# Kernel tuning notes

Hardware: AMD Instinct MI355X
Metric: run time of the kernel (lower is better)

Reference implementation:

```python
import jax, jax.numpy as jnp
import numpy as np

N_NODES = 100000
N_EDGES = 1600000
D_FEAT = 64


def setup_inputs() -> dict:
    key = jax.random.key(0)
    k1, k2, k3 = jax.random.split(key, 3)
    x = jax.random.normal(k1, (N_NODES, D_FEAT), dtype=jnp.float32)
    edge_index = jax.random.randint(k2, (2, N_EDGES), 0, N_NODES, dtype=jnp.int64)
    edge_attr = jax.random.uniform(k3, (N_EDGES,), dtype=jnp.float32)
    return {"x": x, "edge_index": edge_index, "edge_attr": edge_attr}


def reference(x, edge_index, edge_attr):
    # out[row[i]] += exp(-edge_attr[i]) * x[col[i]]  for every edge i
    row, col = edge_index[0], edge_index[1]
    B = jnp.exp(-edge_attr)                      # [E] per-edge scalar kernel
    msgs = B[:, None] * x[col]                   # [E, D] gather + scale
    out = jax.ops.segment_sum(msgs, row, num_segments=N_NODES)  # scatter-add
    return out
```

## Files before the change

kernel.cpp:

```cpp
#include <hip/hip_runtime.h>
#include <math.h>

#define N_NODES_C 100000
#define D_FEAT 64

#define NB_F 512
#define FB_SHIFT 9
#define FB_MASK (NB_F - 1)
#define LMAX 256
#define CAP_E 4096
#define COL_BITS 17
#define COL_MASK17 0x1FFFF
#define NB_AGG 512
#define AGG_ITERS 8

__global__ void spline_scatter_atomic(const float* __restrict__ x,
                                      const int* __restrict__ row_idx,
                                      const int* __restrict__ col_idx,
                                      const float* __restrict__ edge_attr,
                                      float* __restrict__ out,
                                      int n_edges) {
    long long t = (long long)blockIdx.x * blockDim.x + threadIdx.x;
    int e = (int)(t >> 6);
    int f = (int)(t & 63);
    if (e >= n_edges) return;
    int r = row_idx[e];
    int c = col_idx[e];
    float w = expf(-edge_attr[e]);
    atomicAdd(&out[(long long)r * D_FEAT + f], w * x[(long long)c * D_FEAT + f]);
}


__global__ void hist_kernel(const int* __restrict__ row_idx, int* __restrict__ counts,
                            int n_edges) {
    int e = blockIdx.x * blockDim.x + threadIdx.x;
    if (e < n_edges) atomicAdd(&counts[row_idx[e]], 1);
}

__global__ void scan_kernel(const int* __restrict__ counts, int* __restrict__ start,
                            int* __restrict__ cursor, int n) {
    __shared__ int wave_sums[16];
    __shared__ int carry_s;
    const int tid = threadIdx.x;
    const int lane = tid & 63;
    const int wid = tid >> 6;
    if (tid == 0) carry_s = 0;
    __syncthreads();
    for (int base = 0; base < n; base += 1024) {
        int i = base + tid;
        int v = (i < n) ? counts[i] : 0;
        int inc = v;
        #pragma unroll
        for (int d = 1; d < 64; d <<= 1) {
            int t = __shfl_up(inc, d, 64);
            if (lane >= d) inc += t;
        }
        if (lane == 63) wave_sums[wid] = inc;
        __syncthreads();
        if (tid == 0) {
            int s = carry_s;
            #pragma unroll
            for (int k = 0; k < 16; ++k) { int t = wave_sums[k]; wave_sums[k] = s; s += t; }
            carry_s = s;
        }
        __syncthreads();
        int excl = inc - v + wave_sums[wid];
        if (i < n) { start[i] = excl; cursor[i] = excl; }
        __syncthreads();
    }
    if (tid == 0) start[n] = carry_s;
}

__global__ void bucket_kernel(const int* __restrict__ row_idx,
                              const int* __restrict__ col_idx,
                              const float* __restrict__ edge_attr,
                              int* __restrict__ cursor,
                              int2* __restrict__ colw,
                              int n_edges) {
    int e = blockIdx.x * blockDim.x + threadIdx.x;
    if (e >= n_edges) return;
    int r = row_idx[e];
    int c = col_idx[e];
    float w = expf(-edge_attr[e]);
    int pos = atomicAdd(&cursor[r], 1);
    colw[pos] = make_int2(c, __float_as_int(w));
}

__global__ void gather_accum_kernel(const float* __restrict__ x,
                                    const int* __restrict__ start,
                                    const int2* __restrict__ colw,
                                    float* __restrict__ out,
                                    int n_nodes) {
    int node = blockIdx.x * (blockDim.x >> 6) + (threadIdx.x >> 6);
    int lane = threadIdx.x & 63;
    if (node >= n_nodes) return;
    int b = start[node];
    int e = start[node + 1];
    float acc = 0.0f;
    int j = b;
    for (; j + 3 < e; j += 4) {
        int2 c0 = colw[j], c1 = colw[j + 1], c2 = colw[j + 2], c3 = colw[j + 3];
        acc += __int_as_float(c0.y) * x[(size_t)c0.x * D_FEAT + lane];
        acc += __int_as_float(c1.y) * x[(size_t)c1.x * D_FEAT + lane];
        acc += __int_as_float(c2.y) * x[(size_t)c2.x * D_FEAT + lane];
        acc += __int_as_float(c3.y) * x[(size_t)c3.x * D_FEAT + lane];
    }
    for (; j < e; ++j) {
        int2 c0 = colw[j];
        acc += __int_as_float(c0.y) * x[(size_t)c0.x * D_FEAT + lane];
    }
    out[(size_t)node * D_FEAT + lane] = acc;
}


__global__ void init_cursor_kernel(int* __restrict__ ccursor) {
    int i = blockIdx.x * blockDim.x + threadIdx.x;
    if (i < NB_F) ccursor[i] = i * CAP_E;
}

__global__ __launch_bounds__(512) void agg_scatter2_kernel(const int* __restrict__ row,
                                                           const int* __restrict__ col,
                                                           const float* __restrict__ attr,
                                                           int* __restrict__ ccursor,
                                                           int2* __restrict__ cw,
                                                           int n_edges, int chunk) {
    __shared__ int h[NB_F];
    __shared__ int gbase[NB_F];
    __shared__ int lcur[NB_F];
    const int tid = threadIdx.x;
    const int base = blockIdx.x * chunk;
    const int end = min(base + chunk, n_edges);
    h[tid] = 0;
    lcur[tid] = 0;
    __syncthreads();
    int rc[AGG_ITERS];
    #pragma unroll
    for (int k = 0; k < AGG_ITERS; ++k) {
        int e = base + k * 512 + tid;
        rc[k] = (e < end) ? row[e] : -1;
        if (rc[k] >= 0) atomicAdd(&h[rc[k] & FB_MASK], 1);
    }
    __syncthreads();
    {
        int c = h[tid];
        gbase[tid] = c ? atomicAdd(&ccursor[tid], c) : 0;
    }
    __syncthreads();
    #pragma unroll
    for (int k = 0; k < AGG_ITERS; ++k) {
        int e = base + k * 512 + tid;
        int r = rc[k];
        if (r >= 0) {
            int b = r & FB_MASK;
            float w = expf(-attr[e]);
            int p = gbase[b] + atomicAdd(&lcur[b], 1);
            if (p < (b + 1) * CAP_E)
                cw[p] = make_int2(col[e] | ((r >> FB_SHIFT) << COL_BITS),
                                  __float_as_int(w));
        }
    }
}

__global__ __launch_bounds__(1024) void bucket_fused2_kernel(const float* __restrict__ x,
                                                             const int2* __restrict__ cw,
                                                             const int* __restrict__ ccursor,
                                                             float* __restrict__ out,
                                                             int n_nodes) {
    __shared__ int2 sorted[CAP_E];
    __shared__ int lhist[LMAX];
    __shared__ int lbase[LMAX];
    __shared__ int lcur[LMAX];
    __shared__ int wsum[4];
    const int b = blockIdx.x;
    const int tid = threadIdx.x;
    const int lane = tid & 63;
    const int wid = tid >> 6;
    const int beg = b * CAP_E;
    int end = ccursor[b];
    if (end > beg + CAP_E) end = beg + CAP_E;
    const int n = end - beg;

    if (tid < LMAX) lhist[tid] = 0;
    __syncthreads();

    int2 my[CAP_E / 1024];
    #pragma unroll
    for (int k = 0; k < CAP_E / 1024; ++k) {
        int i = tid + k * 1024;
        if (i < n) {
            int2 d = cw[beg + i];
            my[k] = d;
            atomicAdd(&lhist[d.x >> COL_BITS], 1);
        }
    }
    __syncthreads();

    int v = 0, inc = 0;
    if (tid < LMAX) {
        v = lhist[tid];
        inc = v;
        #pragma unroll
        for (int d = 1; d < 64; d <<= 1) {
            int t = __shfl_up(inc, d, 64);
            if (lane >= d) inc += t;
        }
        if (lane == 63) wsum[wid] = inc;
    }
    __syncthreads();
    if (tid == 0) {
        int s = 0;
        #pragma unroll
        for (int k = 0; k < 4; ++k) { int t = wsum[k]; wsum[k] = s; s += t; }
    }
    __syncthreads();
    if (tid < LMAX) {
        int excl = inc - v + wsum[wid];
        lbase[tid] = excl;
        lcur[tid] = excl;
    }
    __syncthreads();

    #pragma unroll
    for (int k = 0; k < CAP_E / 1024; ++k) {
        int i = tid + k * 1024;
        if (i < n) {
            int2 d = my[k];
            int ln = d.x >> COL_BITS;
            int p = atomicAdd(&lcur[ln], 1);
            sorted[p] = make_int2(d.x & COL_MASK17, d.y);
        }
    }
    __syncthreads();

    for (int t2 = 0; t2 < 16; ++t2) {
        int ln = t2 * 16 + wid;
        int node = b + (ln << FB_SHIFT);
        if (node >= n_nodes) break;
        int s = lbase[ln];
        int e2 = (ln + 1 < LMAX) ? lbase[ln + 1] : n;
        float acc = 0.0f;
        int j = s;
        for (; j + 8 <= e2; j += 8) {
            #pragma unroll
            for (int k = 0; k < 8; ++k) {
                int2 d = sorted[j + k];
                acc += __int_as_float(d.y) * x[(size_t)d.x * D_FEAT + lane];
            }
        }
        {
            int rem = e2 - j;
            #pragma unroll
            for (int k = 0; k < 7; ++k) {
                if (k < rem) {
                    int2 d = sorted[j + k];
                    acc += __int_as_float(d.y) * x[(size_t)d.x * D_FEAT + lane];
                }
            }
        }
        out[(size_t)node * D_FEAT + lane] = acc;
    }
}

extern "C" void kernel_launch(void* const* d_in, const int* in_sizes, int n_in,
                              void* d_out, int out_size, void* d_ws, size_t ws_size,
                              hipStream_t stream) {
    const float* x    = (const float*)d_in[0];
    const int*   eidx = (const int*)d_in[1];
    const float* attr = (const float*)d_in[2];
    float*       out  = (float*)d_out;

    const int n_edges = in_sizes[2];
    const int n_nodes = N_NODES_C;
    const int* row = eidx;
    const int* col = eidx + n_edges;

    size_t off_cw   = 0;
    size_t off_ccur = off_cw + (size_t)NB_F * CAP_E * sizeof(int2);
    size_t ws_needed_new = off_ccur + (size_t)NB_F * sizeof(int);

    const int chunk = (n_edges + NB_AGG - 1) / NB_AGG;
    const double mean_fill = (double)n_edges / (double)NB_F;
    bool cap_ok = (mean_fill + 12.0 * sqrt(mean_fill) + 128.0) <= (double)CAP_E;
    cap_ok = cap_ok && (chunk <= 512 * AGG_ITERS);
    cap_ok = cap_ok && (n_nodes <= NB_F * LMAX);

    if (ws_size >= ws_needed_new && cap_ok) {
        char* ws = (char*)d_ws;
        int2* cw      = (int2*)(ws + off_cw);
        int*  ccursor = (int*)(ws + off_ccur);

        init_cursor_kernel<<<(NB_F + 255) / 256, 256, 0, stream>>>(ccursor);
        agg_scatter2_kernel<<<NB_AGG, 512, 0, stream>>>(row, col, attr, ccursor, cw,
                                                        n_edges, chunk);
        bucket_fused2_kernel<<<NB_F, 1024, 0, stream>>>(x, cw, ccursor, out, n_nodes);
        return;
    }

    size_t l_off_colw   = 0;
    size_t l_off_counts = l_off_colw + (size_t)n_edges * sizeof(int2);
    size_t l_off_start  = l_off_counts + (size_t)n_nodes * sizeof(int);
    size_t l_off_cursor = l_off_start + (size_t)(n_nodes + 1) * sizeof(int);
    size_t ws_needed_old = l_off_cursor + (size_t)n_nodes * sizeof(int);

    if (ws_size >= ws_needed_old) {
        char* ws = (char*)d_ws;
        int2* colw   = (int2*)(ws + l_off_colw);
        int*  counts = (int*)(ws + l_off_counts);
        int*  start  = (int*)(ws + l_off_start);
        int*  cursor = (int*)(ws + l_off_cursor);

        hipMemsetAsync(counts, 0, (size_t)n_nodes * sizeof(int), stream);

        const int eb = (n_edges + 255) / 256;
        hist_kernel<<<eb, 256, 0, stream>>>(row, counts, n_edges);
        scan_kernel<<<1, 1024, 0, stream>>>(counts, start, cursor, n_nodes);
        bucket_kernel<<<eb, 256, 0, stream>>>(row, col, attr, cursor, colw, n_edges);

        const int waves_per_block = 4;
        const int nb = (n_nodes + waves_per_block - 1) / waves_per_block;
        gather_accum_kernel<<<nb, 256, 0, stream>>>(x, start, colw, out, n_nodes);
        return;
    }

    hipMemsetAsync(out, 0, (size_t)out_size * sizeof(float), stream);
    const long long total = (long long)n_edges * 64;
    const int blocks = (int)((total + 255) / 256);
    spline_scatter_atomic<<<blocks, 256, 0, stream>>>(x, row, col, attr, out, n_edges);
}
```

Measured before the change: 164.0 us.

## Pad bucket cursors and vectorize gather with float4 per 16-lane node group

Bucket cursors are spread to one per 64-byte stride, so atomics on different buckets no longer contend on the same cache line. The gather phase now gives each node 16 lanes that load float4 rows, instead of one wavefront per node with scalar loads. This cuts the number of load instructions and handles four nodes per wavefront at once. Adding __launch_bounds__(1024, 8) may limit registers, and the bounds check moves so that out-of-range nodes still compute but do not store.

Measured after the change: 178.3 us. 8.7% more time.

```diff
diff --git a/kernel.cpp b/kernel.cpp
--- a/kernel.cpp
+++ b/kernel.cpp
@@ -13,6 +13,7 @@
 #define COL_MASK17 0x1FFFF
 #define NB_AGG 512
 #define AGG_ITERS 8
+#define CCS 16
 
 __global__ void spline_scatter_atomic(const float* __restrict__ x,
                                       const int* __restrict__ row_idx,
@@ -115,7 +116,7 @@
 
 __global__ void init_cursor_kernel(int* __restrict__ ccursor) {
     int i = blockIdx.x * blockDim.x + threadIdx.x;
-    if (i < NB_F) ccursor[i] = i * CAP_E;
+    if (i < NB_F) ccursor[i * CCS] = i * CAP_E;
 }
 
 __global__ __launch_bounds__(512) void agg_scatter2_kernel(const int* __restrict__ row,
@@ -143,7 +144,7 @@
     __syncthreads();
     {
         int c = h[tid];
-        gbase[tid] = c ? atomicAdd(&ccursor[tid], c) : 0;
+        gbase[tid] = c ? atomicAdd(&ccursor[tid * CCS], c) : 0;
     }
     __syncthreads();
     #pragma unroll
@@ -161,11 +162,11 @@
     }
 }
 
-__global__ __launch_bounds__(1024) void bucket_fused2_kernel(const float* __restrict__ x,
-                                                             const int2* __restrict__ cw,
-                                                             const int* __restrict__ ccursor,
-                                                             float* __restrict__ out,
-                                                             int n_nodes) {
+__global__ __launch_bounds__(1024, 8) void bucket_fused3_kernel(const float* __restrict__ x,
+                                                                const int2* __restrict__ cw,
+                                                                const int* __restrict__ ccursor,
+                                                                float* __restrict__ out,
+                                                                int n_nodes) {
     __shared__ int2 sorted[CAP_E];
     __shared__ int lhist[LMAX];
     __shared__ int lbase[LMAX];
@@ -176,7 +177,7 @@
     const int lane = tid & 63;
     const int wid = tid >> 6;
     const int beg = b * CAP_E;
-    int end = ccursor[b];
+    int end = ccursor[b * CCS];
     if (end > beg + CAP_E) end = beg + CAP_E;
     const int n = end - beg;
 
@@ -232,32 +233,42 @@
     }
     __syncthreads();
 
-    for (int t2 = 0; t2 < 16; ++t2) {
-        int ln = t2 * 16 + wid;
+    const int sl = tid & 15;
+    const int grp = tid >> 4;
+    #pragma unroll
+    for (int t2 = 0; t2 < 4; ++t2) {
+        int ln = t2 * 64 + grp;
         int node = b + (ln << FB_SHIFT);
-        if (node >= n_nodes) break;
         int s = lbase[ln];
         int e2 = (ln + 1 < LMAX) ? lbase[ln + 1] : n;
-        float acc = 0.0f;
+        float4 acc = make_float4(0.f, 0.f, 0.f, 0.f);
         int j = s;
-        for (; j + 8 <= e2; j += 8) {
+        for (; j + 4 <= e2; j += 4) {
             #pragma unroll
-            for (int k = 0; k < 8; ++k) {
+            for (int k = 0; k < 4; ++k) {
                 int2 d = sorted[j + k];
-                acc += __int_as_float(d.y) * x[(size_t)d.x * D_FEAT + lane];
+                const float4 xv = *(const float4*)(x + ((size_t)d.x << 6) + (sl << 2));
+                float w = __int_as_float(d.y);
+                acc.x += w * xv.x;
+                acc.y += w * xv.y;
+                acc.z += w * xv.z;
+                acc.w += w * xv.w;
             }
         }
-        {
-            int rem = e2 - j;
-            #pragma unroll
-            for (int k = 0; k < 7; ++k) {
-                if (k < rem) {
-                    int2 d = sorted[j + k];
-                    acc += __int_as_float(d.y) * x[(size_t)d.x * D_FEAT + lane];
-                }
+        #pragma unroll
+        for (int k = 0; k < 3; ++k) {
+            if (j + k < e2) {
+                int2 d = sorted[j + k];
+                const float4 xv = *(const float4*)(x + ((size_t)d.x << 6) + (sl << 2));
+                float w = __int_as_float(d.y);
+                acc.x += w * xv.x;
+                acc.y += w * xv.y;
+                acc.z += w * xv.z;
+                acc.w += w * xv.w;
             }
         }
-        out[(size_t)node * D_FEAT + lane] = acc;
+        if (node < n_nodes)
+            *(float4*)(out + ((size_t)node << 6) + (sl << 2)) = acc;
     }
 }
 
@@ -276,7 +287,7 @@
 
     size_t off_cw   = 0;
     size_t off_ccur = off_cw + (size_t)NB_F * CAP_E * sizeof(int2);
-    size_t ws_needed_new = off_ccur + (size_t)NB_F * sizeof(int);
+    size_t ws_needed_new = off_ccur + (size_t)NB_F * CCS * sizeof(int);
 
     const int chunk = (n_edges + NB_AGG - 1) / NB_AGG;
     const double mean_fill = (double)n_edges / (double)NB_F;
@@ -292,7 +303,7 @@
         init_cursor_kernel<<<(NB_F + 255) / 256, 256, 0, stream>>>(ccursor);
         agg_scatter2_kernel<<<NB_AGG, 512, 0, stream>>>(row, col, attr, ccursor, cw,
                                                         n_edges, chunk);
-        bucket_fused2_kernel<<<NB_F, 1024, 0, stream>>>(x, cw, ccursor, out, n_nodes);
+        bucket_fused3_kernel<<<NB_F, 1024, 0, stream>>>(x, cw, ccursor, out, n_nodes);
         return;
     }
 
```
